# Kernel tuning notes

Hardware: AMD Instinct MI355X
Metric: run time of the kernel (lower is better)

The kernel has to match this reference:

```python
import jax, jax.numpy as jnp
import numpy as np
from jax import lax

FILTER_SIZE = 3
C_IN = 128
C_OUT = 256
PAD = 1
STRIDE = 1


def setup_inputs() -> dict:
    key = jax.random.key(0)
    k1, k2 = jax.random.split(key)
    prev_a = jax.random.normal(k1, (32, 56, 56, C_IN), dtype=jnp.float32)
    # filter_w initialized ~ N(0, 1) as in the original tf.random.normal
    filter_w = jax.random.normal(k2, (FILTER_SIZE, FILTER_SIZE, C_IN, C_OUT), dtype=jnp.float32)
    filter_b = jnp.zeros((1, 1, 1, C_OUT), dtype=jnp.float32)
    return {"prev_a": prev_a, "filter_w": filter_w, "filter_b": filter_b}


def reference(prev_a, filter_w, filter_b):
    # NHWC input, HWIO filter -> NHWC output; same math as the nested-loop conv:
    # z[i,h,w,c] = sum(prev_a_pad[i, h*s:h*s+f, w*s:w*s+f, :] * W[:,:,:,c]) + b[c]
    z = lax.conv_general_dilated(
        prev_a,
        filter_w,
        window_strides=(STRIDE, STRIDE),
        padding=[(PAD, PAD), (PAD, PAD)],
        dimension_numbers=("NHWC", "HWIO", "NHWC"),
    )
    z = z + filter_b  # bias broadcast over (m, H, W)
    return jax.nn.relu(z)
```

## Files before the change

kernel.cpp:

```cpp
#include <hip/hip_runtime.h>
#include <hip/hip_bf16.h>


#define NIMG 32
#define HH 56
#define WW 56
#define PH 58
#define PW 58
#define CIN 128
#define COUT 256
#define KTOT 1152
#define PAD_ELEMS (NIMG * PH * PW * CIN)

#define BM 224
#define BK 64
#define NT (KTOT / BK)
#define NBLK ((NIMG * HH * WW) / BM)

#define AREG_SZ 7168
#define BREG_BASE 28672
#define BREG_SZ 8192

typedef __attribute__((ext_vector_type(8))) short bf16x8;
typedef __attribute__((ext_vector_type(4))) short s16x4;
typedef __attribute__((ext_vector_type(4))) float f32x4;

__device__ __forceinline__ short f2bf(float x) {
    union { __hip_bfloat16 b; short s; } u;
    u.b = __float2bfloat16(x);
    return u.s;
}

typedef const void __attribute__((address_space(1)))* gas1_t;
typedef void __attribute__((address_space(3)))* las3_t;
__device__ __forceinline__ void async16(short* lds_p, const short* g) {
    __builtin_amdgcn_global_load_lds((gas1_t)g, (las3_t)lds_p, 16, 0, 0);
}

__global__ __launch_bounds__(256) void pack_input(const float* __restrict__ in,
                                                  short* __restrict__ pad) {
    const int tid  = blockIdx.x * 256 + threadIdx.x;
    const int flat = tid * 8;
    const int c8   = flat & (CIN - 1);
    const int rest = flat >> 7;
    const int iw   = rest % PW;
    const int r2   = rest / PW;
    const int ih   = r2 % PH;
    const int img  = r2 / PH;
    bf16x8 v = (bf16x8)0;
    if (ih >= 1 && ih <= HH && iw >= 1 && iw <= WW) {
        const float* p = in + (((size_t)(img * HH + ih - 1) * WW + (iw - 1)) * CIN + c8);
        const float4 x0 = *(const float4*)p;
        const float4 x1 = *(const float4*)(p + 4);
        v.s0 = f2bf(x0.x); v.s1 = f2bf(x0.y); v.s2 = f2bf(x0.z); v.s3 = f2bf(x0.w);
        v.s4 = f2bf(x1.x); v.s5 = f2bf(x1.y); v.s6 = f2bf(x1.z); v.s7 = f2bf(x1.w);
    }
    *(bf16x8*)(pad + flat) = v;
}

__global__ __launch_bounds__(256) void pack_wgt(const float* __restrict__ w,
                                                short* __restrict__ wt) {
    __shared__ short tile[32][33];
    const int k0 = blockIdx.x * 32;
    const int n0 = blockIdx.y * 32;
    const int t  = threadIdx.x;
    {
        const int kl  = t >> 3;
        const int nl4 = (t & 7) * 4;
        const float4 x = *(const float4*)(w + (size_t)(k0 + kl) * COUT + n0 + nl4);
        tile[kl][nl4 + 0] = f2bf(x.x);
        tile[kl][nl4 + 1] = f2bf(x.y);
        tile[kl][nl4 + 2] = f2bf(x.z);
        tile[kl][nl4 + 3] = f2bf(x.w);
    }
    __syncthreads();
    {
        const int nl  = t >> 3;
        const int kl4 = (t & 7) * 4;
        s16x4 v;
        v.x = tile[kl4 + 0][nl];
        v.y = tile[kl4 + 1][nl];
        v.z = tile[kl4 + 2][nl];
        v.w = tile[kl4 + 3][nl];
        *(s16x4*)(wt + (size_t)(n0 + nl) * KTOT + k0 + kl4) = v;
    }
}

#define FENCE() asm volatile("" ::: "memory")
#define BARRIER() do { FENCE(); __builtin_amdgcn_s_barrier(); FENCE(); } while (0)
#define VMWAIT(N) asm volatile("s_waitcnt vmcnt(" #N ")" ::: "memory")

__global__ __launch_bounds__(512, 2) void conv_mfma(const short* __restrict__ apad,
                                                    const short* __restrict__ bwt,
                                                    const float* __restrict__ bias,
                                                    float* __restrict__ out) {
    __shared__ short lds[61440];

    const int t  = threadIdx.x;
    const int l  = t & 63;
    const int w  = t >> 6;
    const int wm = w >> 2;
    const int wn = w & 3;
    const int fr = l & 15;
    const int fq = l >> 4;

    const int laneoff = fr * 32 + ((fq ^ ((fr >> 1) & 3))) * 8;
    const int afb = wm * 3584;
    const int bfb = wn * 2048;
    const int kcs = (t & 3) ^ ((t >> 3) & 3);

    const int bid = blockIdx.x;
    const int swz = (bid & 7) * (NBLK / 8) + (bid >> 3);
    const int m0  = swz * BM;

    const int r0 = t >> 2;
    int abase0, abase1;
    {
        int m = m0 + r0;
        int img = m / (HH * WW), rem = m - img * (HH * WW);
        int oh = rem / WW, ow = rem - oh * WW;
        abase0 = ((img * PH + oh) * PW + ow) * CIN;
        if (t < 384) {
            m = m0 + r0 + 128;
            img = m / (HH * WW); rem = m - img * (HH * WW);
            oh = rem / WW; ow = rem - oh * WW;
            abase1 = ((img * PH + oh) * PW + ow) * CIN;
        } else {
            abase1 = abase0;
        }
    }
    const int a2lds = (w < 6) ? (4096 + w * 512) : (w * 512);
    const int bbase0 = r0 * KTOT;
    const int bbase1 = (r0 + 128) * KTOT;

    f32x4 acc[7][4];
#pragma unroll
    for (int i = 0; i < 7; ++i)
#pragma unroll
        for (int j = 0; j < 4; ++j) { f32x4 z = {0.f, 0.f, 0.f, 0.f}; acc[i][j] = z; }

    bf16x8 M0a[4], M0b[4], M1a[3], M1b[3], Ba[4], Bb[4];

#define STAGE_A(KT, KH) do {                                                  \
        const int _tap = (KT) >> 1;                                           \
        const int _fh  = (_tap * 11) >> 5;                   \
        const int _fw  = _tap - 3 * _fh;                                      \
        const int _off = (_fh * PW + _fw) * CIN + ((KT) & 1) * 64             \
                         + (KH) * 32 + kcs * 8;                               \
        short* _l = lds + ((((KT) & 1) << 1) + (KH)) * AREG_SZ;               \
        async16(_l + w * 512, apad + abase0 + _off);                          \
        async16(_l + a2lds,   apad + abase1 + _off);                          \
    } while (0)

#define STAGE_B(KT, KH) do {                                                  \
        const int _off = (KT) * 64 + (KH) * 32 + kcs * 8;                     \
        short* _l = lds + BREG_BASE + ((((KT) & 1) << 1) + (KH)) * BREG_SZ;   \
        async16(_l + w * 512,        bwt + bbase0 + _off);                    \
        async16(_l + 4096 + w * 512, bwt + bbase1 + _off);                    \
    } while (0)

#define RD_M0B(M0, BF, REG) do {                                              \
        const short* _a = lds + (REG) * AREG_SZ;                              \
        const short* _b = lds + BREG_BASE + (REG) * BREG_SZ;                  \
        _Pragma("unroll")                                                     \
        for (int _i = 0; _i < 4; ++_i)                                        \
            (M0)[_i] = *(const bf16x8*)(_a + afb + _i * 512 + laneoff);       \
        _Pragma("unroll")                                                     \
        for (int _j = 0; _j < 4; ++_j)                                        \
            (BF)[_j] = *(const bf16x8*)(_b + bfb + _j * 512 + laneoff);       \
    } while (0)

#define RD_M1(M1, REG) do {                                                   \
        const short* _a = lds + (REG) * AREG_SZ;                              \
        _Pragma("unroll")                                                     \
        for (int _i = 0; _i < 3; ++_i)                                        \
            (M1)[_i] = *(const bf16x8*)(_a + afb + 2048 + _i * 512 + laneoff);\
    } while (0)

#define MM0(M0, BF) do {                                                      \
        __builtin_amdgcn_s_setprio(1);                                        \
        _Pragma("unroll")                                                     \
        for (int _i = 0; _i < 4; ++_i)                                        \
            _Pragma("unroll")                                                 \
            for (int _j = 0; _j < 4; ++_j)                                    \
                acc[_i][_j] = __builtin_amdgcn_mfma_f32_16x16x32_bf16(        \
                    (M0)[_i], (BF)[_j], acc[_i][_j], 0, 0, 0);                \
        __builtin_amdgcn_s_setprio(0);                                        \
    } while (0)

#define MM1(M1, BF) do {                                                      \
        __builtin_amdgcn_s_setprio(1);                                        \
        _Pragma("unroll")                                                     \
        for (int _i = 0; _i < 3; ++_i)                                        \
            _Pragma("unroll")                                                 \
            for (int _j = 0; _j < 4; ++_j)                                    \
                acc[4 + _i][_j] = __builtin_amdgcn_mfma_f32_16x16x32_bf16(    \
                    (M1)[_i], (BF)[_j], acc[4 + _i][_j], 0, 0, 0);            \
        __builtin_amdgcn_s_setprio(0);                                        \
    } while (0)

    STAGE_A(0, 0); STAGE_B(0, 0);
    STAGE_A(0, 1); STAGE_B(0, 1);
    STAGE_A(1, 0); STAGE_B(1, 0);
    VMWAIT(8);
    BARRIER();
    RD_M0B(M0a, Ba, 0);

#pragma unroll 1
    for (int kt = 0; kt < NT - 2; kt += 2) {
        STAGE_A(kt + 1, 1); MM0(M0a, Ba); VMWAIT(6); RD_M1(M1a, 0);      BARRIER();
        STAGE_B(kt + 1, 1); MM1(M1a, Ba);            RD_M0B(M0b, Bb, 1); BARRIER();
        STAGE_A(kt + 2, 0); MM0(M0b, Bb); VMWAIT(6); RD_M1(M1b, 1);      BARRIER();
        STAGE_B(kt + 2, 0); MM1(M1b, Bb);            RD_M0B(M0a, Ba, 2); BARRIER();
        STAGE_A(kt + 2, 1); MM0(M0a, Ba); VMWAIT(6); RD_M1(M1a, 2);      BARRIER();
        STAGE_B(kt + 2, 1); MM1(M1a, Ba);            RD_M0B(M0b, Bb, 3); BARRIER();
        STAGE_A(kt + 3, 0); MM0(M0b, Bb); VMWAIT(6); RD_M1(M1b, 3);      BARRIER();
        STAGE_B(kt + 3, 0); MM1(M1b, Bb);            RD_M0B(M0a, Ba, 0); BARRIER();
    }

    STAGE_A(NT - 1, 1); MM0(M0a, Ba); VMWAIT(6); RD_M1(M1a, 0);      BARRIER();
    STAGE_B(NT - 1, 1); MM1(M1a, Ba);            RD_M0B(M0b, Bb, 1); BARRIER();
    MM0(M0b, Bb); VMWAIT(4); RD_M1(M1b, 1);      BARRIER();
    MM1(M1b, Bb);            RD_M0B(M0a, Ba, 2); BARRIER();
    MM0(M0a, Ba); VMWAIT(0); RD_M1(M1a, 2);      BARRIER();
    MM1(M1a, Ba);            RD_M0B(M0b, Bb, 3); BARRIER();
    MM0(M0b, Bb);            RD_M1(M1b, 3);      BARRIER();
    MM1(M1b, Bb);

#pragma unroll
    for (int j = 0; j < 4; ++j) {
        const int n  = wn * 64 + j * 16 + fr;
        const float bj = bias[n];
#pragma unroll
        for (int i = 0; i < 7; ++i) {
            const int mr = m0 + wm * 112 + i * 16 + fq * 4;
#pragma unroll
            for (int r = 0; r < 4; ++r) {
                const float v = acc[i][j][r] + bj;
                out[(size_t)(mr + r) * COUT + n] = v > 0.f ? v : 0.f;
            }
        }
    }
#undef STAGE_A
#undef STAGE_B
#undef RD_M0B
#undef RD_M1
#undef MM0
#undef MM1
}

extern "C" void kernel_launch(void* const* d_in, const int* in_sizes, int n_in,
                              void* d_out, int out_size, void* d_ws, size_t ws_size,
                              hipStream_t stream) {
    const float* in   = (const float*)d_in[0];
    const float* wgt  = (const float*)d_in[1];
    const float* bias = (const float*)d_in[2];
    float* out = (float*)d_out;

    short* pad = (short*)d_ws;
    short* wt  = (short*)d_ws + PAD_ELEMS;

    pack_input<<<PAD_ELEMS / 8 / 256, 256, 0, stream>>>(in, pad);
    pack_wgt<<<dim3(KTOT / 32, COUT / 32), 256, 0, stream>>>(wgt, wt);

    conv_mfma<<<NBLK, 512, 0, stream>>>(pad, wt, bias, out);
}
```

Before: 200.6 us.

## Restructure conv main loop into unified 4-stage K=32 pipeline with full-tile MFMA phases

Replaces the split A/B staging and two half-tile MFMA phases with a single STAGE macro that loads both A and B slices for one 32-wide K chunk into a 4-deep LDS ring. Each step reads all seven A fragments and four B fragments, then issues the full 7x4 MFMA block, with one barrier per step instead of two. The aim is to cut barrier count and simplify overlap of LDS reads with MFMA. In exchange it holds more fragment registers (two full A sets) and leaves a shorter gap between the LDS read and the ring-slot overwrite, which may add register pressure or stalls.

```diff
diff --git a/kernel.cpp b/kernel.cpp
--- a/kernel.cpp
+++ b/kernel.cpp
@@ -139,93 +139,63 @@
 #pragma unroll
         for (int j = 0; j < 4; ++j) { f32x4 z = {0.f, 0.f, 0.f, 0.f}; acc[i][j] = z; }
 
-    bf16x8 M0a[4], M0b[4], M1a[3], M1b[3], Ba[4], Bb[4];
-
-#define STAGE_A(KT, KH) do {                                                  \
-        const int _tap = (KT) >> 1;                                           \
-        const int _fh  = (_tap * 11) >> 5;                   \
-        const int _fw  = _tap - 3 * _fh;                                      \
-        const int _off = (_fh * PW + _fw) * CIN + ((KT) & 1) * 64             \
-                         + (KH) * 32 + kcs * 8;                               \
-        short* _l = lds + ((((KT) & 1) << 1) + (KH)) * AREG_SZ;               \
-        async16(_l + w * 512, apad + abase0 + _off);                          \
-        async16(_l + a2lds,   apad + abase1 + _off);                          \
+    bf16x8 Aa[7], Ab[7], Ba[4], Bb[4];
+
+#define STAGE(K) do {                                                         \
+        const int _tap  = (K) >> 2;                                           \
+        const int _fh   = (_tap * 11) >> 5;                  \
+        const int _fw   = _tap - 3 * _fh;                                     \
+        const int _aoff = (_fh * PW + _fw) * CIN + ((K) & 3) * 32 + kcs * 8;  \
+        const int _boff = (K) * 32 + kcs * 8;                                 \
+        short* _la = lds + ((K) & 3) * AREG_SZ;                               \
+        short* _lb = lds + BREG_BASE + ((K) & 3) * BREG_SZ;                   \
+        async16(_la + w * 512, apad + abase0 + _aoff);                        \
+        async16(_la + a2lds,   apad + abase1 + _aoff);                        \
+        async16(_lb + w * 512,        bwt + bbase0 + _boff);                  \
+        async16(_lb + 4096 + w * 512, bwt + bbase1 + _boff);                  \
     } while (0)
 
-#define STAGE_B(KT, KH) do {                                                  \
-        const int _off = (KT) * 64 + (KH) * 32 + kcs * 8;                     \
-        short* _l = lds + BREG_BASE + ((((KT) & 1) << 1) + (KH)) * BREG_SZ;   \
-        async16(_l + w * 512,        bwt + bbase0 + _off);                    \
-        async16(_l + 4096 + w * 512, bwt + bbase1 + _off);                    \
-    } while (0)
-
-#define RD_M0B(M0, BF, REG) do {                                              \
-        const short* _a = lds + (REG) * AREG_SZ;                              \
-        const short* _b = lds + BREG_BASE + (REG) * BREG_SZ;                  \
+#define RD(AF, BF, R) do {                                                    \
+        const short* _a = lds + (R) * AREG_SZ;                                \
+        const short* _b = lds + BREG_BASE + (R) * BREG_SZ;                    \
         _Pragma("unroll")                                                     \
-        for (int _i = 0; _i < 4; ++_i)                                        \
-            (M0)[_i] = *(const bf16x8*)(_a + afb + _i * 512 + laneoff);       \
+        for (int _i = 0; _i < 7; ++_i)                                        \
+            (AF)[_i] = *(const bf16x8*)(_a + afb + _i * 512 + laneoff);       \
         _Pragma("unroll")                                                     \
         for (int _j = 0; _j < 4; ++_j)                                        \
             (BF)[_j] = *(const bf16x8*)(_b + bfb + _j * 512 + laneoff);       \
     } while (0)
 
-#define RD_M1(M1, REG) do {                                                   \
-        const short* _a = lds + (REG) * AREG_SZ;                              \
-        _Pragma("unroll")                                                     \
-        for (int _i = 0; _i < 3; ++_i)                                        \
-            (M1)[_i] = *(const bf16x8*)(_a + afb + 2048 + _i * 512 + laneoff);\
-    } while (0)
-
-#define MM0(M0, BF) do {                                                      \
+#define MM(AF, BF) do {                                                       \
         __builtin_amdgcn_s_setprio(1);                                        \
         _Pragma("unroll")                                                     \
-        for (int _i = 0; _i < 4; ++_i)                                        \
+        for (int _i = 0; _i < 7; ++_i)                                        \
             _Pragma("unroll")                                                 \
             for (int _j = 0; _j < 4; ++_j)                                    \
                 acc[_i][_j] = __builtin_amdgcn_mfma_f32_16x16x32_bf16(        \
-                    (M0)[_i], (BF)[_j], acc[_i][_j], 0, 0, 0);                \
+                    (AF)[_i], (BF)[_j], acc[_i][_j], 0, 0, 0);                \
         __builtin_amdgcn_s_setprio(0);                                        \
     } while (0)
 
-#define MM1(M1, BF) do {                                                      \
-        __builtin_amdgcn_s_setprio(1);                                        \
-        _Pragma("unroll")                                                     \
-        for (int _i = 0; _i < 3; ++_i)                                        \
-            _Pragma("unroll")                                                 \
-            for (int _j = 0; _j < 4; ++_j)                                    \
-                acc[4 + _i][_j] = __builtin_amdgcn_mfma_f32_16x16x32_bf16(    \
-                    (M1)[_i], (BF)[_j], acc[4 + _i][_j], 0, 0, 0);            \
-        __builtin_amdgcn_s_setprio(0);                                        \
-    } while (0)
-
-    STAGE_A(0, 0); STAGE_B(0, 0);
-    STAGE_A(0, 1); STAGE_B(0, 1);
-    STAGE_A(1, 0); STAGE_B(1, 0);
+    STAGE(0); STAGE(1); STAGE(2); STAGE(3);
     VMWAIT(8);
     BARRIER();
-    RD_M0B(M0a, Ba, 0);
+    RD(Aa, Ba, 0);
+    BARRIER();
 
 #pragma unroll 1
-    for (int kt = 0; kt < NT - 2; kt += 2) {
-        STAGE_A(kt + 1, 1); MM0(M0a, Ba); VMWAIT(6); RD_M1(M1a, 0);      BARRIER();
-        STAGE_B(kt + 1, 1); MM1(M1a, Ba);            RD_M0B(M0b, Bb, 1); BARRIER();
-        STAGE_A(kt + 2, 0); MM0(M0b, Bb); VMWAIT(6); RD_M1(M1b, 1);      BARRIER();
-        STAGE_B(kt + 2, 0); MM1(M1b, Bb);            RD_M0B(M0a, Ba, 2); BARRIER();
-        STAGE_A(kt + 2, 1); MM0(M0a, Ba); VMWAIT(6); RD_M1(M1a, 2);      BARRIER();
-        STAGE_B(kt + 2, 1); MM1(M1a, Ba);            RD_M0B(M0b, Bb, 3); BARRIER();
-        STAGE_A(kt + 3, 0); MM0(M0b, Bb); VMWAIT(6); RD_M1(M1b, 3);      BARRIER();
-        STAGE_B(kt + 3, 0); MM1(M1b, Bb);            RD_M0B(M0a, Ba, 0); BARRIER();
-    }
-
-    STAGE_A(NT - 1, 1); MM0(M0a, Ba); VMWAIT(6); RD_M1(M1a, 0);      BARRIER();
-    STAGE_B(NT - 1, 1); MM1(M1a, Ba);            RD_M0B(M0b, Bb, 1); BARRIER();
-    MM0(M0b, Bb); VMWAIT(4); RD_M1(M1b, 1);      BARRIER();
-    MM1(M1b, Bb);            RD_M0B(M0a, Ba, 2); BARRIER();
-    MM0(M0a, Ba); VMWAIT(0); RD_M1(M1a, 2);      BARRIER();
-    MM1(M1a, Ba);            RD_M0B(M0b, Bb, 3); BARRIER();
-    MM0(M0b, Bb);            RD_M1(M1b, 3);      BARRIER();
-    MM1(M1b, Bb);
+    for (int j = 0; j < 8; ++j) {
+        const int p0 = j * 4;
+        STAGE(p0 + 4); RD(Ab, Bb, 1); MM(Aa, Ba); VMWAIT(8); BARRIER();
+        STAGE(p0 + 5); RD(Aa, Ba, 2); MM(Ab, Bb); VMWAIT(8); BARRIER();
+        STAGE(p0 + 6); RD(Ab, Bb, 3); MM(Aa, Ba); VMWAIT(8); BARRIER();
+        STAGE(p0 + 7); RD(Aa, Ba, 0); MM(Ab, Bb); VMWAIT(8); BARRIER();
+    }
+
+    RD(Ab, Bb, 1); MM(Aa, Ba); VMWAIT(4); BARRIER();
+    RD(Aa, Ba, 2); MM(Ab, Bb); VMWAIT(0); BARRIER();
+    RD(Ab, Bb, 3); MM(Aa, Ba); BARRIER();
+    MM(Ab, Bb);
 
 #pragma unroll
     for (int j = 0; j < 4; ++j) {
@@ -241,12 +211,9 @@
             }
         }
     }
-#undef STAGE_A
-#undef STAGE_B
-#undef RD_M0B
-#undef RD_M1
-#undef MM0
-#undef MM1
+#undef STAGE
+#undef RD
+#undef MM
 }
 
 extern "C" void kernel_launch(void* const* d_in, const int* in_sizes, int n_in,
```

New measurement: 202.0 us. Within noise of the previous version (+0.7%).
